# Optimization experiments

Measured on AMD Instinct MI355X. Metric: run time of the kernel, lower is better.

## Reference

```python
import jax, jax.numpy as jnp
import numpy as np

IN_DIM = 512
C_OUT = IN_DIM // 8  # 64
B, H, W = 8, 128, 128


def setup_inputs() -> dict:
    key = jax.random.key(0)
    ks = jax.random.split(key, 6)
    x = jax.random.normal(ks[0], (B, IN_DIM, H, W), dtype=jnp.float32)
    # 1x1 conv weights stored as [out_ch, in_ch] matrices (kernel size 1)
    qkv_w = jax.random.normal(ks[1], (3 * C_OUT, IN_DIM), dtype=jnp.float32) * (1.0 / np.sqrt(IN_DIM))
    qkv_b = jax.random.normal(ks[2], (3 * C_OUT,), dtype=jnp.float32) * 0.01
    out_w = jax.random.normal(ks[3], (IN_DIM, C_OUT), dtype=jnp.float32) * (1.0 / np.sqrt(C_OUT))
    out_b = jax.random.normal(ks[4], (IN_DIM,), dtype=jnp.float32) * 0.01
    # gamma is init to 0 in torch; use a small nonzero value so both paths are exercised
    gamma = jnp.asarray(0.5, dtype=jnp.float32)
    return {"x": x, "qkv_w": qkv_w, "qkv_b": qkv_b, "out_w": out_w, "out_b": out_b, "gamma": gamma}


def reference(x, qkv_w, qkv_b, out_w, out_b, gamma):
    # qkv_conv: 1x1 conv == channel matmul
    qkv = jnp.einsum('bchw,oc->bohw', x, qkv_w) + qkv_b[None, :, None, None]
    q, k, v = jnp.split(qkv, 3, axis=1)  # each [B, C', H, W]

    # Horizontal branch: per column w, channel-channel attention contracting over H
    energy_h = jnp.einsum('bqhw,bkhw->bwqk', q, k)          # [B, W, C', C']
    attn_h = jax.nn.softmax(energy_h, axis=-1)
    out_h = jnp.einsum('bwqk,bkhw->bqhw', attn_h, v)        # [B, C', H, W]

    # Vertical branch: per row h, channel-channel attention contracting over W
    energy_v = jnp.einsum('bqhw,bkhw->bhqk', q, k)          # [B, H, C', C']
    attn_v = jax.nn.softmax(energy_v, axis=-1)
    out_v = jnp.einsum('bhqk,bkhw->bqhw', attn_v, v)        # [B, C', H, W]

    out = gamma * (out_h + out_v)
    out = jnp.einsum('bchw,oc->bohw', out, out_w) + out_b[None, :, None, None]
    return out + x
```

## Files before the change

kernel.cpp:

```cpp
#include <hip/hip_runtime.h>


typedef _Float16 f16;
typedef _Float16 f16x4 __attribute__((ext_vector_type(4)));
typedef _Float16 f16x8 __attribute__((ext_vector_type(8)));
typedef float f32x4 __attribute__((ext_vector_type(4)));

#define MFMA16(a, b, c) __builtin_amdgcn_mfma_f32_16x16x32_f16(a, b, c, 0, 0, 0)

constexpr int CIN = 512;
constexpr int COUT = 64;
constexpr int HW = 128;
constexpr int P = HW * HW;
constexpr int QKV_CH = 192;

__global__ __launch_bounds__(256) void qkv_gemm(
    const float* __restrict__ x, const float* __restrict__ w,
    const float* __restrict__ bias, f16* __restrict__ qkv)
{
  __shared__ __attribute__((aligned(16))) f16 Wl[QKV_CH * 40];
  __shared__ __attribute__((aligned(16))) f16 Xt[128 * 40];
  const int p0 = blockIdx.x * 128;
  const int b = blockIdx.y;
  const float* xb = x + (size_t)b * CIN * P;
  const int t = threadIdx.x;
  const int lane = t & 63, wv = t >> 6;
  const int quad = lane >> 4, l15 = lane & 15;
  const int wm = (wv >> 1) * 32, wn = (wv & 1) * 64;

  f32x4 acc[3][4][2] = {};
  for (int k0 = 0; k0 < CIN; k0 += 32) {
    for (int it = 0; it < 6; ++it) {
      int c = t + it * 256;
      int row = c >> 3, c4 = (c & 7) * 4;
      const float4 v = *(const float4*)(w + (size_t)row * CIN + k0 + c4);
      f16* d = &Wl[row * 40 + c4];
      d[0] = (f16)v.x; d[1] = (f16)v.y; d[2] = (f16)v.z; d[3] = (f16)v.w;
    }
    for (int it = 0; it < 4; ++it) {
      int c = t + it * 256;
      int kr = c >> 5, p4 = (c & 31) * 4;
      const float4 v = *(const float4*)(xb + (size_t)(k0 + kr) * P + p0 + p4);
      float vv[4] = {v.x, v.y, v.z, v.w};
#pragma unroll
      for (int j = 0; j < 4; ++j) {
        int p = p4 + j;
        int kc = kr ^ (((p >> 3) & 3) << 3);
        Xt[p * 40 + kc] = (f16)vv[j];
      }
    }
    __syncthreads();
    f16x8 xf[4];
#pragma unroll
    for (int ps = 0; ps < 4; ++ps) {
      int pr = wn + ps * 16 + l15;
      int kb = (quad * 8) ^ (((pr >> 3) & 3) << 3);
      xf[ps] = *(const f16x8*)&Xt[pr * 40 + kb];
    }
#pragma unroll
    for (int mt = 0; mt < 3; ++mt) {
      f16x8 wf[2];
#pragma unroll
      for (int ms = 0; ms < 2; ++ms)
        wf[ms] = *(const f16x8*)&Wl[(mt * 64 + wm + ms * 16 + l15) * 40 + quad * 8];
#pragma unroll
      for (int ps = 0; ps < 4; ++ps)
#pragma unroll
        for (int ms = 0; ms < 2; ++ms)
          acc[mt][ps][ms] = MFMA16(xf[ps], wf[ms], acc[mt][ps][ms]);
    }
    __syncthreads();
  }
  f16* ob = qkv + (size_t)b * QKV_CH * P;
#pragma unroll
  for (int mt = 0; mt < 3; ++mt) {
#pragma unroll
    for (int ms = 0; ms < 2; ++ms) {
      int m = mt * 64 + wm + ms * 16 + l15;
      float bi = bias[m];
#pragma unroll
      for (int ps = 0; ps < 4; ++ps) {
        int p = p0 + wn + ps * 16 + quad * 4;
        f16x4 tmp;
#pragma unroll
        for (int r = 0; r < 4; ++r) tmp[r] = (f16)(acc[mt][ps][ms][r] + bi);
        *(f16x4*)(ob + (size_t)m * P + p) = tmp;
      }
    }
  }
}

__global__ __launch_bounds__(256) void transpose_hw(
    const f16* __restrict__ in, f16* __restrict__ out)
{
  __shared__ __attribute__((aligned(16))) f16 T[64 * 72];
  const size_t plane = blockIdx.x;
  const int r0 = blockIdx.y * 64, c0 = blockIdx.z * 64;
  const f16* ip = in + plane * P;
  f16* op = out + plane * P;
  const int t = threadIdx.x;
  for (int it = 0; it < 2; ++it) {
    int c = t + it * 256;
    int row = c >> 3, c8 = (c & 7) * 8;
    *(f16x8*)&T[row * 72 + c8] =
        *(const f16x8*)(ip + (size_t)(r0 + row) * HW + c0 + c8);
  }
  __syncthreads();
  for (int it = 0; it < 2; ++it) {
    int c = t + it * 256;
    int wr = c >> 3, h8 = (c & 7) * 8;
    f16 tmp[8];
#pragma unroll
    for (int j = 0; j < 8; ++j) tmp[j] = T[(h8 + j) * 72 + wr];
    *(f16x8*)(op + (size_t)(c0 + wr) * HW + r0 + h8) = *(const f16x8*)tmp;
  }
}

__global__ __launch_bounds__(256, 4) void cc_attn(
    const f16* __restrict__ qkvT, const f16* __restrict__ qkvN,
    f16* __restrict__ outT, f16* __restrict__ outN)
{
  __shared__ __attribute__((aligned(16))) f16 smem[64 * 136 + 128 * 72];
  f16* Kl = smem;
  f16* Vt = smem + 64 * 136;
  f16* Al = smem;
  f16* Ol = smem;
  const int s = blockIdx.x, b = blockIdx.y;
  const f16* src = blockIdx.z ? qkvN : qkvT;
  f16* dst = blockIdx.z ? outN : outT;
  const f16* base = src + (size_t)b * QKV_CH * P + (size_t)s * HW;
  const int t = threadIdx.x;
  const int lane = t & 63, wv = t >> 6;
  const int quad = lane >> 4, l15 = lane & 15;
  const int m0 = wv * 16;

  f16x8 aq[4];
#pragma unroll
  for (int kk = 0; kk < 4; ++kk)
    aq[kk] = *(const f16x8*)(base + (size_t)(m0 + l15) * P + kk * 32 + quad * 8);

  for (int it = 0; it < 4; ++it) {
    int c = t + it * 256;
    int row = c >> 4, c8 = (c & 15) * 8;
    *(f16x8*)&Kl[row * 136 + c8] =
        *(const f16x8*)(base + (size_t)(64 + row) * P + c8);
    f16x8 v = *(const f16x8*)(base + (size_t)(128 + row) * P + c8);
#pragma unroll
    for (int j = 0; j < 8; ++j) {
      int h = c8 + j;
      int kc = row ^ (((h >> 3) & 7) << 3);
      Vt[h * 72 + kc] = v[j];
    }
  }
  __syncthreads();

  f32x4 e[4] = {};
#pragma unroll
  for (int kk = 0; kk < 4; ++kk) {
#pragma unroll
    for (int nt = 0; nt < 4; ++nt) {
      f16x8 bk = *(const f16x8*)&Kl[(nt * 16 + l15) * 136 + kk * 32 + quad * 8];
      e[nt] = MFMA16(aq[kk], bk, e[nt]);
    }
  }
  float pr[4][4];
  float rinv[4];
#pragma unroll
  for (int r = 0; r < 4; ++r) {
    float mx = fmaxf(fmaxf(e[0][r], e[1][r]), fmaxf(e[2][r], e[3][r]));
    for (int off = 1; off < 16; off <<= 1) mx = fmaxf(mx, __shfl_xor(mx, off));
    float sm = 0.f;
#pragma unroll
    for (int nt = 0; nt < 4; ++nt) {
      float pv = __expf(e[nt][r] - mx);
      pr[nt][r] = pv;
      sm += pv;
    }
    for (int off = 1; off < 16; off <<= 1) sm += __shfl_xor(sm, off);
    rinv[r] = 1.0f / sm;
  }
  __syncthreads();

#pragma unroll
  for (int nt = 0; nt < 4; ++nt)
#pragma unroll
    for (int r = 0; r < 4; ++r)
      Al[(m0 + quad * 4 + r) * 72 + nt * 16 + l15] = (f16)(pr[nt][r] * rinv[r]);

  f32x4 o[8] = {};
#pragma unroll
  for (int kk = 0; kk < 2; ++kk) {
    f16x8 ap = *(const f16x8*)&Al[(m0 + l15) * 72 + kk * 32 + quad * 8];
#pragma unroll
    for (int nt = 0; nt < 8; ++nt) {
      int hr = nt * 16 + l15;
      int kb = (kk * 32 + quad * 8) ^ (((hr >> 3) & 7) << 3);
      f16x8 bv = *(const f16x8*)&Vt[hr * 72 + kb];
      o[nt] = MFMA16(ap, bv, o[nt]);
    }
  }
  __syncthreads();

#pragma unroll
  for (int nt = 0; nt < 8; ++nt)
#pragma unroll
    for (int r = 0; r < 4; ++r) {
      int row = m0 + quad * 4 + r;
      int col = nt * 16 + l15;
      Ol[row * 136 + (col ^ ((row & 15) << 3))] = (f16)o[nt][r];
    }
  f16* db = dst + (size_t)b * COUT * P + (size_t)s * HW;
#pragma unroll
  for (int it = 0; it < 4; ++it) {
    int c = lane + it * 64;
    int row = m0 + (c >> 4);
    int c8 = (c & 15) * 8;
    f16x8 vv = *(const f16x8*)&Ol[row * 136 + (c8 ^ ((row & 15) << 3))];
    *(f16x8*)(db + (size_t)row * P + c8) = vv;
  }
}

__global__ __launch_bounds__(256) void out_proj(
    const f16* __restrict__ ah, const f16* __restrict__ av,
    const float* __restrict__ w, const float* __restrict__ bias,
    const float* __restrict__ gamma_p, const float* __restrict__ x,
    float* __restrict__ out)
{
  __shared__ __attribute__((aligned(16))) f16 St[128 * 72];
  const int p0 = blockIdx.x * 128;
  const int b = blockIdx.y;
  const int t = threadIdx.x;
  const int lane = t & 63, wv = t >> 6;
  const int quad = lane >> 4, l15 = lane & 15;
  const int wm = (wv >> 1) * 32, wn = (wv & 1) * 64;

  const size_t abase = (size_t)b * COUT * P + p0;
  for (int it = 0; it < 4; ++it) {
    int c = t + it * 256;
    int k = c >> 4, p8 = (c & 15) * 8;
    f16x8 a = *(const f16x8*)(ah + abase + (size_t)k * P + p8);
    f16x8 vv = *(const f16x8*)(av + abase + (size_t)k * P + p8);
#pragma unroll
    for (int j = 0; j < 8; ++j) {
      int p = p8 + j;
      int kc = k ^ (((p >> 3) & 7) << 3);
      St[p * 72 + kc] = (f16)(a[j] + vv[j]);
    }
  }
  __syncthreads();

  f16x8 sf[2][4];
#pragma unroll
  for (int kk = 0; kk < 2; ++kk)
#pragma unroll
    for (int ps = 0; ps < 4; ++ps) {
      int pr2 = wn + ps * 16 + l15;
      int kb = (kk * 32 + quad * 8) ^ (((pr2 >> 3) & 7) << 3);
      sf[kk][ps] = *(const f16x8*)&St[pr2 * 72 + kb];
    }

  const float g = *gamma_p;
  const float* xb = x + (size_t)b * CIN * P;
  float* ob = out + (size_t)b * CIN * P;

  for (int mt = 0; mt < 8; ++mt) {
    const int m0 = mt * 64;
    f16x8 wf[2][2];
#pragma unroll
    for (int ms = 0; ms < 2; ++ms) {
      const float* wr = w + (size_t)(m0 + wm + ms * 16 + l15) * COUT;
#pragma unroll
      for (int kk = 0; kk < 2; ++kk) {
        const float4 w0 = *(const float4*)(wr + kk * 32 + quad * 8);
        const float4 w1 = *(const float4*)(wr + kk * 32 + quad * 8 + 4);
        f16x8 f;
        f[0] = (f16)w0.x; f[1] = (f16)w0.y; f[2] = (f16)w0.z; f[3] = (f16)w0.w;
        f[4] = (f16)w1.x; f[5] = (f16)w1.y; f[6] = (f16)w1.z; f[7] = (f16)w1.w;
        wf[kk][ms] = f;
      }
    }
    f32x4 acc[4][2] = {};
#pragma unroll
    for (int kk = 0; kk < 2; ++kk)
#pragma unroll
      for (int ps = 0; ps < 4; ++ps)
#pragma unroll
        for (int ms = 0; ms < 2; ++ms)
          acc[ps][ms] = MFMA16(sf[kk][ps], wf[kk][ms], acc[ps][ms]);
#pragma unroll
    for (int ms = 0; ms < 2; ++ms) {
      int m = m0 + wm + ms * 16 + l15;
      float bi = bias[m];
#pragma unroll
      for (int ps = 0; ps < 4; ++ps) {
        int p = p0 + wn + ps * 16 + quad * 4;
        size_t idx = (size_t)m * P + p;
        const float4 xv = *(const float4*)(xb + idx);
        float4 ov;
        ov.x = g * acc[ps][ms][0] + bi + xv.x;
        ov.y = g * acc[ps][ms][1] + bi + xv.y;
        ov.z = g * acc[ps][ms][2] + bi + xv.z;
        ov.w = g * acc[ps][ms][3] + bi + xv.w;
        *(float4*)(ob + idx) = ov;
      }
    }
  }
}

extern "C" void kernel_launch(void* const* d_in, const int* in_sizes, int n_in,
                              void* d_out, int out_size, void* d_ws,
                              size_t ws_size, hipStream_t stream)
{
  (void)in_sizes; (void)n_in; (void)out_size; (void)ws_size;
  const float* x = (const float*)d_in[0];
  const float* qkv_w = (const float*)d_in[1];
  const float* qkv_b = (const float*)d_in[2];
  const float* out_w = (const float*)d_in[3];
  const float* out_b = (const float*)d_in[4];
  const float* gamma = (const float*)d_in[5];
  float* out = (float*)d_out;

  char* ws = (char*)d_ws;
  const size_t QKV_BYTES = (size_t)8 * QKV_CH * P * sizeof(f16);
  const size_t ATT_BYTES = (size_t)8 * COUT * P * sizeof(f16);
  f16* qkv  = (f16*)ws;
  f16* qkvT = (f16*)(ws + QKV_BYTES);
  f16* ahT  = (f16*)(ws + 2 * QKV_BYTES);
  f16* ahN  = (f16*)(ws + 2 * QKV_BYTES + ATT_BYTES);
  f16* avN  = (f16*)(ws + 2 * QKV_BYTES + 2 * ATT_BYTES);

  qkv_gemm<<<dim3(128, 8), 256, 0, stream>>>(x, qkv_w, qkv_b, qkv);
  transpose_hw<<<dim3(8 * QKV_CH, 2, 2), 256, 0, stream>>>(qkv, qkvT);
  cc_attn<<<dim3(128, 8, 2), 256, 0, stream>>>(qkvT, qkv, ahT, avN);
  transpose_hw<<<dim3(8 * COUT, 2, 2), 256, 0, stream>>>(ahT, ahN);
  out_proj<<<dim3(128, 8), 256, 0, stream>>>(ahN, avN, out_w, out_b, gamma,
                                             x, out);
}
```

Baseline: 601.7 us.

## Fuse transposes into QKV GEMM and out-projection, pre-convert weights to fp16

Both standalone transpose kernels are removed. The QKV GEMM now tiles pixels as 8x16 spatial blocks and writes the result in both normal and transposed layouts through a swizzled LDS staging buffer. The out-projection reads the transposed horizontal-branch output directly, also using spatial tiles. Weights are converted to fp16 once in a small prep kernel, and the GEMM register-prefetches the next K slice while computing the current one. This cuts two launches and a full round trip of intermediate tensors through global memory. In exchange it adds strided transposed writes and reads plus extra LDS synchronisation.

```diff
diff --git a/kernel.cpp b/kernel.cpp
--- a/kernel.cpp
+++ b/kernel.cpp
@@ -14,13 +14,33 @@
 constexpr int P = HW * HW;
 constexpr int QKV_CH = 192;
 
+__global__ __launch_bounds__(256) void prep_w(
+    const float* __restrict__ qw, const float* __restrict__ ow,
+    f16* __restrict__ qw16, f16* __restrict__ ow16)
+{
+  int i = blockIdx.x * 256 + threadIdx.x;
+  const float* src;
+  f16* dst;
+  int off;
+  if (i < 24576) { src = qw; dst = qw16; off = i; }
+  else           { src = ow; dst = ow16; off = i - 24576; }
+  const float4 v = *(const float4*)(src + (size_t)off * 4);
+  f16x4 o;
+  o[0] = (f16)v.x; o[1] = (f16)v.y; o[2] = (f16)v.z; o[3] = (f16)v.w;
+  *(f16x4*)(dst + (size_t)off * 4) = o;
+}
+
 __global__ __launch_bounds__(256) void qkv_gemm(
-    const float* __restrict__ x, const float* __restrict__ w,
-    const float* __restrict__ bias, f16* __restrict__ qkv)
-{
-  __shared__ __attribute__((aligned(16))) f16 Wl[QKV_CH * 40];
-  __shared__ __attribute__((aligned(16))) f16 Xt[128 * 40];
-  const int p0 = blockIdx.x * 128;
+    const float* __restrict__ x, const f16* __restrict__ w16,
+    const float* __restrict__ bias, f16* __restrict__ qkv,
+    f16* __restrict__ qkvT)
+{
+  __shared__ __attribute__((aligned(16))) f16 pool[QKV_CH * 40 + 128 * 40];
+  f16* Wl = pool;
+  f16* Xt = pool + QKV_CH * 40;
+  f16* Cl = pool;
+  const int bx = blockIdx.x;
+  const int h0 = (bx >> 3) * 8, w0 = (bx & 7) * 16;
   const int b = blockIdx.y;
   const float* xb = x + (size_t)b * CIN * P;
   const int t = threadIdx.x;
@@ -28,28 +48,46 @@
   const int quad = lane >> 4, l15 = lane & 15;
   const int wm = (wv >> 1) * 32, wn = (wv & 1) * 64;
 
+  f16x8 wvr[3];
+  float4 xvr[4];
+#define LOADW(s)                                                          \
+  _Pragma("unroll") for (int it = 0; it < 3; ++it) {                      \
+    int c = t + it * 256;                                                 \
+    wvr[it] = *(const f16x8*)(w16 + (size_t)(c >> 2) * CIN + (s) * 32 +   \
+                              (c & 3) * 8);                               \
+  }
+#define LOADX(s)                                                          \
+  _Pragma("unroll") for (int it = 0; it < 4; ++it) {                      \
+    int c = t + it * 256;                                                 \
+    int kr = c >> 5, sub = c & 31;                                        \
+    xvr[it] = *(const float4*)(xb + (size_t)((s) * 32 + kr) * P +         \
+                               (h0 + (sub >> 2)) * 128 + w0 + (sub & 3) * 4); \
+  }
+
+  LOADW(0);
+  LOADX(0);
   f32x4 acc[3][4][2] = {};
-  for (int k0 = 0; k0 < CIN; k0 += 32) {
-    for (int it = 0; it < 6; ++it) {
+  for (int s = 0; s < 16; ++s) {
+#pragma unroll
+    for (int it = 0; it < 3; ++it) {
       int c = t + it * 256;
-      int row = c >> 3, c4 = (c & 7) * 4;
-      const float4 v = *(const float4*)(w + (size_t)row * CIN + k0 + c4);
-      f16* d = &Wl[row * 40 + c4];
-      d[0] = (f16)v.x; d[1] = (f16)v.y; d[2] = (f16)v.z; d[3] = (f16)v.w;
-    }
+      *(f16x8*)&Wl[(c >> 2) * 40 + (c & 3) * 8] = wvr[it];
+    }
+#pragma unroll
     for (int it = 0; it < 4; ++it) {
       int c = t + it * 256;
-      int kr = c >> 5, p4 = (c & 31) * 4;
-      const float4 v = *(const float4*)(xb + (size_t)(k0 + kr) * P + p0 + p4);
-      float vv[4] = {v.x, v.y, v.z, v.w};
+      int kr = c >> 5, sub = c & 31;
+      int pb = (sub >> 2) * 16 + (sub & 3) * 4;
+      float vv[4] = {xvr[it].x, xvr[it].y, xvr[it].z, xvr[it].w};
 #pragma unroll
       for (int j = 0; j < 4; ++j) {
-        int p = p4 + j;
+        int p = pb + j;
         int kc = kr ^ (((p >> 3) & 3) << 3);
         Xt[p * 40 + kc] = (f16)vv[j];
       }
     }
     __syncthreads();
+    if (s < 15) { LOADW(s + 1); LOADX(s + 1); }
     f16x8 xf[4];
 #pragma unroll
     for (int ps = 0; ps < 4; ++ps) {
@@ -71,48 +109,53 @@
     }
     __syncthreads();
   }
-  f16* ob = qkv + (size_t)b * QKV_CH * P;
+#undef LOADW
+#undef LOADX
+
+  f16* obN = qkv + (size_t)b * QKV_CH * P;
+  f16* obT = qkvT + (size_t)b * QKV_CH * P;
 #pragma unroll
   for (int mt = 0; mt < 3; ++mt) {
 #pragma unroll
     for (int ms = 0; ms < 2; ++ms) {
-      int m = mt * 64 + wm + ms * 16 + l15;
-      float bi = bias[m];
+      int ml = wm + ms * 16 + l15;
+      float bi = bias[mt * 64 + ml];
 #pragma unroll
       for (int ps = 0; ps < 4; ++ps) {
-        int p = p0 + wn + ps * 16 + quad * 4;
-        f16x4 tmp;
-#pragma unroll
-        for (int r = 0; r < 4; ++r) tmp[r] = (f16)(acc[mt][ps][ms][r] + bi);
-        *(f16x4*)(ob + (size_t)m * P + p) = tmp;
+        int pst = wn + ps * 16 + quad * 4;
+        int col = (((pst >> 3) ^ (ml & 7)) << 3) + (pst & 7);
+        f16x4 tv;
+#pragma unroll
+        for (int r = 0; r < 4; ++r) tv[r] = (f16)(acc[mt][ps][ms][r] + bi);
+        *(f16x4*)&Cl[ml * 136 + col] = tv;
       }
     }
-  }
-}
-
-__global__ __launch_bounds__(256) void transpose_hw(
-    const f16* __restrict__ in, f16* __restrict__ out)
-{
-  __shared__ __attribute__((aligned(16))) f16 T[64 * 72];
-  const size_t plane = blockIdx.x;
-  const int r0 = blockIdx.y * 64, c0 = blockIdx.z * 64;
-  const f16* ip = in + plane * P;
-  f16* op = out + plane * P;
-  const int t = threadIdx.x;
-  for (int it = 0; it < 2; ++it) {
-    int c = t + it * 256;
-    int row = c >> 3, c8 = (c & 7) * 8;
-    *(f16x8*)&T[row * 72 + c8] =
-        *(const f16x8*)(ip + (size_t)(r0 + row) * HW + c0 + c8);
-  }
-  __syncthreads();
-  for (int it = 0; it < 2; ++it) {
-    int c = t + it * 256;
-    int wr = c >> 3, h8 = (c & 7) * 8;
-    f16 tmp[8];
-#pragma unroll
-    for (int j = 0; j < 8; ++j) tmp[j] = T[(h8 + j) * 72 + wr];
-    *(f16x8*)(op + (size_t)(c0 + wr) * HW + r0 + h8) = *(const f16x8*)tmp;
+    __syncthreads();
+#pragma unroll
+    for (int it = 0; it < 4; ++it) {
+      int c = t + it * 256;
+      int ml = c >> 4, sub = c & 15;
+      int hh = sub >> 1, w8 = (sub & 1) * 8;
+      int pst = hh * 16 + w8;
+      int col = (((pst >> 3) ^ (ml & 7)) << 3);
+      f16x8 rd = *(const f16x8*)&Cl[ml * 136 + col];
+      *(f16x8*)(obN + (size_t)(mt * 64 + ml) * P + (h0 + hh) * 128 + w0 + w8) = rd;
+    }
+#pragma unroll
+    for (int it = 0; it < 4; ++it) {
+      int c = t + it * 256;
+      int ml = c >> 4, ww = c & 15;
+      f16 tmp[8];
+#pragma unroll
+      for (int hh = 0; hh < 8; ++hh) {
+        int p = hh * 16 + ww;
+        int col = (((p >> 3) ^ (ml & 7)) << 3) + (p & 7);
+        tmp[hh] = Cl[ml * 136 + col];
+      }
+      *(f16x8*)(obT + (size_t)(mt * 64 + ml) * P + (size_t)(w0 + ww) * 128 + h0) =
+          *(const f16x8*)tmp;
+    }
+    __syncthreads();
   }
 }
 
@@ -221,30 +264,42 @@
 }
 
 __global__ __launch_bounds__(256) void out_proj(
-    const f16* __restrict__ ah, const f16* __restrict__ av,
-    const float* __restrict__ w, const float* __restrict__ bias,
+    const f16* __restrict__ ahT, const f16* __restrict__ av,
+    const f16* __restrict__ w16, const float* __restrict__ bias,
     const float* __restrict__ gamma_p, const float* __restrict__ x,
     float* __restrict__ out)
 {
   __shared__ __attribute__((aligned(16))) f16 St[128 * 72];
-  const int p0 = blockIdx.x * 128;
+  const int bx = blockIdx.x;
+  const int h0 = (bx >> 3) * 8, w0 = (bx & 7) * 16;
   const int b = blockIdx.y;
   const int t = threadIdx.x;
   const int lane = t & 63, wv = t >> 6;
   const int quad = lane >> 4, l15 = lane & 15;
   const int wm = (wv >> 1) * 32, wn = (wv & 1) * 64;
 
-  const size_t abase = (size_t)b * COUT * P + p0;
+  const size_t abase = (size_t)b * COUT * P;
   for (int it = 0; it < 4; ++it) {
     int c = t + it * 256;
-    int k = c >> 4, p8 = (c & 15) * 8;
-    f16x8 a = *(const f16x8*)(ah + abase + (size_t)k * P + p8);
-    f16x8 vv = *(const f16x8*)(av + abase + (size_t)k * P + p8);
+    int k = c >> 4, sub = c & 15;
+    int hh = sub >> 1, w8 = (sub & 1) * 8;
+    f16x8 vv = *(const f16x8*)(av + abase + (size_t)k * P + (h0 + hh) * 128 + w0 + w8);
 #pragma unroll
     for (int j = 0; j < 8; ++j) {
-      int p = p8 + j;
-      int kc = k ^ (((p >> 3) & 7) << 3);
-      St[p * 72 + kc] = (f16)(a[j] + vv[j]);
+      int p = hh * 16 + w8 + j;
+      St[p * 72 + (k ^ (((p >> 3) & 7) << 3))] = vv[j];
+    }
+  }
+  __syncthreads();
+  for (int it = 0; it < 4; ++it) {
+    int c = t + it * 256;
+    int k = c >> 4, ww = c & 15;
+    f16x8 vv = *(const f16x8*)(ahT + abase + (size_t)k * P + (size_t)(w0 + ww) * 128 + h0);
+#pragma unroll
+    for (int j = 0; j < 8; ++j) {
+      int p = j * 16 + ww;
+      int idx = p * 72 + (k ^ (((p >> 3) & 7) << 3));
+      St[idx] = St[idx] + vv[j];
     }
   }
   __syncthreads();
@@ -268,16 +323,10 @@
     f16x8 wf[2][2];
 #pragma unroll
     for (int ms = 0; ms < 2; ++ms) {
-      const float* wr = w + (size_t)(m0 + wm + ms * 16 + l15) * COUT;
-#pragma unroll
-      for (int kk = 0; kk < 2; ++kk) {
-        const float4 w0 = *(const float4*)(wr + kk * 32 + quad * 8);
-        const float4 w1 = *(const float4*)(wr + kk * 32 + quad * 8 + 4);
-        f16x8 f;
-        f[0] = (f16)w0.x; f[1] = (f16)w0.y; f[2] = (f16)w0.z; f[3] = (f16)w0.w;
-        f[4] = (f16)w1.x; f[5] = (f16)w1.y; f[6] = (f16)w1.z; f[7] = (f16)w1.w;
-        wf[kk][ms] = f;
-      }
+      const f16* wr = w16 + (size_t)(m0 + wm + ms * 16 + l15) * COUT;
+#pragma unroll
+      for (int kk = 0; kk < 2; ++kk)
+        wf[kk][ms] = *(const f16x8*)(wr + kk * 32 + quad * 8);
     }
     f32x4 acc[4][2] = {};
 #pragma unroll
@@ -293,8 +342,9 @@
       float bi = bias[m];
 #pragma unroll
       for (int ps = 0; ps < 4; ++ps) {
-        int p = p0 + wn + ps * 16 + quad * 4;
-        size_t idx = (size_t)m * P + p;
+        int pst = wn + ps * 16 + quad * 4;
+        int hh = pst >> 4, ww = pst & 15;
+        size_t idx = (size_t)m * P + (h0 + hh) * 128 + w0 + ww;
         const float4 xv = *(const float4*)(xb + idx);
         float4 ov;
         ov.x = g * acc[ps][ms][0] + bi + xv.x;
@@ -326,13 +376,13 @@
   f16* qkv  = (f16*)ws;
   f16* qkvT = (f16*)(ws + QKV_BYTES);
   f16* ahT  = (f16*)(ws + 2 * QKV_BYTES);
-  f16* ahN  = (f16*)(ws + 2 * QKV_BYTES + ATT_BYTES);
-  f16* avN  = (f16*)(ws + 2 * QKV_BYTES + 2 * ATT_BYTES);
-
-  qkv_gemm<<<dim3(128, 8), 256, 0, stream>>>(x, qkv_w, qkv_b, qkv);
-  transpose_hw<<<dim3(8 * QKV_CH, 2, 2), 256, 0, stream>>>(qkv, qkvT);
+  f16* avN  = (f16*)(ws + 2 * QKV_BYTES + ATT_BYTES);
+  f16* wq16 = (f16*)(ws + 2 * QKV_BYTES + 2 * ATT_BYTES);
+  f16* wo16 = wq16 + (size_t)QKV_CH * CIN;
+
+  prep_w<<<dim3(128), 256, 0, stream>>>(qkv_w, out_w, wq16, wo16);
+  qkv_gemm<<<dim3(128, 8), 256, 0, stream>>>(x, wq16, qkv_b, qkv, qkvT);
   cc_attn<<<dim3(128, 8, 2), 256, 0, stream>>>(qkvT, qkv, ahT, avN);
-  transpose_hw<<<dim3(8 * COUT, 2, 2), 256, 0, stream>>>(ahT, ahN);
-  out_proj<<<dim3(128, 8), 256, 0, stream>>>(ahN, avN, out_w, out_b, gamma,
+  out_proj<<<dim3(128, 8), 256, 0, stream>>>(ahT, avN, wo16, out_b, gamma,
                                              x, out);
 }
```

Measured after the change: 656.9 us. 1.09x slower.

## Pre-convert weights to fp16, prefetch qkv_gemm tiles, shrink out_proj tiles

Applied to the files above, without the earlier changes.

Adds a small kernel that converts both weight matrices to fp16 once per call, so the GEMMs load half-width weights and skip per-tile conversion. qkv_gemm now register-prefetches the next K-slice of weights and x while MFMAs run on the current slice (software pipelining). out_proj is retiled to 64 pixels per block with each wave owning 16 output rows, doubling the grid and setting launch bounds for more occupancy. The cost is an extra kernel launch, some extra workspace, and higher register pressure in qkv_gemm.

```diff
diff --git a/kernel.cpp b/kernel.cpp
--- a/kernel.cpp
+++ b/kernel.cpp
@@ -14,8 +14,24 @@
 constexpr int P = HW * HW;
 constexpr int QKV_CH = 192;
 
+__global__ __launch_bounds__(256) void prep_w(
+    const float* __restrict__ qw, const float* __restrict__ ow,
+    f16* __restrict__ qw16, f16* __restrict__ ow16)
+{
+  int i = blockIdx.x * 256 + threadIdx.x;
+  const float* src;
+  f16* dst;
+  int off;
+  if (i < 24576) { src = qw; dst = qw16; off = i; }
+  else           { src = ow; dst = ow16; off = i - 24576; }
+  const float4 v = *(const float4*)(src + (size_t)off * 4);
+  f16x4 o;
+  o[0] = (f16)v.x; o[1] = (f16)v.y; o[2] = (f16)v.z; o[3] = (f16)v.w;
+  *(f16x4*)(dst + (size_t)off * 4) = o;
+}
+
 __global__ __launch_bounds__(256) void qkv_gemm(
-    const float* __restrict__ x, const float* __restrict__ w,
+    const float* __restrict__ x, const f16* __restrict__ w16,
     const float* __restrict__ bias, f16* __restrict__ qkv)
 {
   __shared__ __attribute__((aligned(16))) f16 Wl[QKV_CH * 40];
@@ -28,20 +44,35 @@
   const int quad = lane >> 4, l15 = lane & 15;
   const int wm = (wv >> 1) * 32, wn = (wv & 1) * 64;
 
+  f16x8 wvr[3];
+  float4 xvr[4];
+#define LOADW(s)                                                          \
+  _Pragma("unroll") for (int it = 0; it < 3; ++it) {                      \
+    int c = t + it * 256;                                                 \
+    wvr[it] = *(const f16x8*)(w16 + (size_t)(c >> 2) * CIN + (s) * 32 +   \
+                              (c & 3) * 8);                               \
+  }
+#define LOADX(s)                                                          \
+  _Pragma("unroll") for (int it = 0; it < 4; ++it) {                      \
+    int c = t + it * 256;                                                 \
+    xvr[it] = *(const float4*)(xb + (size_t)((s) * 32 + (c >> 5)) * P +   \
+                               p0 + (c & 31) * 4);                        \
+  }
+
+  LOADW(0);
+  LOADX(0);
   f32x4 acc[3][4][2] = {};
-  for (int k0 = 0; k0 < CIN; k0 += 32) {
-    for (int it = 0; it < 6; ++it) {
+  for (int s = 0; s < 16; ++s) {
+#pragma unroll
+    for (int it = 0; it < 3; ++it) {
       int c = t + it * 256;
-      int row = c >> 3, c4 = (c & 7) * 4;
-      const float4 v = *(const float4*)(w + (size_t)row * CIN + k0 + c4);
-      f16* d = &Wl[row * 40 + c4];
-      d[0] = (f16)v.x; d[1] = (f16)v.y; d[2] = (f16)v.z; d[3] = (f16)v.w;
-    }
+      *(f16x8*)&Wl[(c >> 2) * 40 + (c & 3) * 8] = wvr[it];
+    }
+#pragma unroll
     for (int it = 0; it < 4; ++it) {
       int c = t + it * 256;
       int kr = c >> 5, p4 = (c & 31) * 4;
-      const float4 v = *(const float4*)(xb + (size_t)(k0 + kr) * P + p0 + p4);
-      float vv[4] = {v.x, v.y, v.z, v.w};
+      float vv[4] = {xvr[it].x, xvr[it].y, xvr[it].z, xvr[it].w};
 #pragma unroll
       for (int j = 0; j < 4; ++j) {
         int p = p4 + j;
@@ -50,6 +81,7 @@
       }
     }
     __syncthreads();
+    if (s < 15) { LOADW(s + 1); LOADX(s + 1); }
     f16x8 xf[4];
 #pragma unroll
     for (int ps = 0; ps < 4; ++ps) {
@@ -71,6 +103,9 @@
     }
     __syncthreads();
   }
+#undef LOADW
+#undef LOADX
+
   f16* ob = qkv + (size_t)b * QKV_CH * P;
 #pragma unroll
   for (int mt = 0; mt < 3; ++mt) {
@@ -220,31 +255,29 @@
   }
 }
 
-__global__ __launch_bounds__(256) void out_proj(
+__global__ __launch_bounds__(256, 5) void out_proj(
     const f16* __restrict__ ah, const f16* __restrict__ av,
-    const float* __restrict__ w, const float* __restrict__ bias,
+    const f16* __restrict__ w16, const float* __restrict__ bias,
     const float* __restrict__ gamma_p, const float* __restrict__ x,
     float* __restrict__ out)
 {
-  __shared__ __attribute__((aligned(16))) f16 St[128 * 72];
-  const int p0 = blockIdx.x * 128;
+  __shared__ __attribute__((aligned(16))) f16 St[64 * 72];
+  const int p0 = blockIdx.x * 64;
   const int b = blockIdx.y;
   const int t = threadIdx.x;
   const int lane = t & 63, wv = t >> 6;
   const int quad = lane >> 4, l15 = lane & 15;
-  const int wm = (wv >> 1) * 32, wn = (wv & 1) * 64;
 
   const size_t abase = (size_t)b * COUT * P + p0;
-  for (int it = 0; it < 4; ++it) {
+  for (int it = 0; it < 2; ++it) {
     int c = t + it * 256;
-    int k = c >> 4, p8 = (c & 15) * 8;
+    int k = c >> 3, p8 = (c & 7) * 8;
     f16x8 a = *(const f16x8*)(ah + abase + (size_t)k * P + p8);
     f16x8 vv = *(const f16x8*)(av + abase + (size_t)k * P + p8);
 #pragma unroll
     for (int j = 0; j < 8; ++j) {
       int p = p8 + j;
-      int kc = k ^ (((p >> 3) & 7) << 3);
-      St[p * 72 + kc] = (f16)(a[j] + vv[j]);
+      St[p * 72 + (k ^ (((p >> 3) & 7) << 3))] = (f16)(a[j] + vv[j]);
     }
   }
   __syncthreads();
@@ -254,7 +287,7 @@
   for (int kk = 0; kk < 2; ++kk)
 #pragma unroll
     for (int ps = 0; ps < 4; ++ps) {
-      int pr2 = wn + ps * 16 + l15;
+      int pr2 = ps * 16 + l15;
       int kb = (kk * 32 + quad * 8) ^ (((pr2 >> 3) & 7) << 3);
       sf[kk][ps] = *(const f16x8*)&St[pr2 * 72 + kb];
     }
@@ -264,45 +297,29 @@
   float* ob = out + (size_t)b * CIN * P;
 
   for (int mt = 0; mt < 8; ++mt) {
-    const int m0 = mt * 64;
-    f16x8 wf[2][2];
-#pragma unroll
-    for (int ms = 0; ms < 2; ++ms) {
-      const float* wr = w + (size_t)(m0 + wm + ms * 16 + l15) * COUT;
-#pragma unroll
-      for (int kk = 0; kk < 2; ++kk) {
-        const float4 w0 = *(const float4*)(wr + kk * 32 + quad * 8);
-        const float4 w1 = *(const float4*)(wr + kk * 32 + quad * 8 + 4);
-        f16x8 f;
-        f[0] = (f16)w0.x; f[1] = (f16)w0.y; f[2] = (f16)w0.z; f[3] = (f16)w0.w;
-        f[4] = (f16)w1.x; f[5] = (f16)w1.y; f[6] = (f16)w1.z; f[7] = (f16)w1.w;
-        wf[kk][ms] = f;
-      }
-    }
-    f32x4 acc[4][2] = {};
+    const int m = mt * 64 + wv * 16 + l15;
+    f16x8 wf[2];
 #pragma unroll
     for (int kk = 0; kk < 2; ++kk)
+      wf[kk] = *(const f16x8*)(w16 + (size_t)m * COUT + kk * 32 + quad * 8);
+    f32x4 acc[4] = {};
+#pragma unroll
+    for (int kk = 0; kk < 2; ++kk)
 #pragma unroll
       for (int ps = 0; ps < 4; ++ps)
-#pragma unroll
-        for (int ms = 0; ms < 2; ++ms)
-          acc[ps][ms] = MFMA16(sf[kk][ps], wf[kk][ms], acc[ps][ms]);
-#pragma unroll
-    for (int ms = 0; ms < 2; ++ms) {
-      int m = m0 + wm + ms * 16 + l15;
-      float bi = bias[m];
-#pragma unroll
-      for (int ps = 0; ps < 4; ++ps) {
-        int p = p0 + wn + ps * 16 + quad * 4;
-        size_t idx = (size_t)m * P + p;
-        const float4 xv = *(const float4*)(xb + idx);
-        float4 ov;
-        ov.x = g * acc[ps][ms][0] + bi + xv.x;
-        ov.y = g * acc[ps][ms][1] + bi + xv.y;
-        ov.z = g * acc[ps][ms][2] + bi + xv.z;
-        ov.w = g * acc[ps][ms][3] + bi + xv.w;
-        *(float4*)(ob + idx) = ov;
-      }
+        acc[ps] = MFMA16(sf[kk][ps], wf[kk], acc[ps]);
+    float bi = bias[m];
+#pragma unroll
+    for (int ps = 0; ps < 4; ++ps) {
+      int p = p0 + ps * 16 + quad * 4;
+      size_t idx = (size_t)m * P + p;
+      const float4 xv = *(const float4*)(xb + idx);
+      float4 ov;
+      ov.x = g * acc[ps][0] + bi + xv.x;
+      ov.y = g * acc[ps][1] + bi + xv.y;
+      ov.z = g * acc[ps][2] + bi + xv.z;
+      ov.w = g * acc[ps][3] + bi + xv.w;
+      *(float4*)(ob + idx) = ov;
     }
   }
 }
@@ -328,11 +345,14 @@
   f16* ahT  = (f16*)(ws + 2 * QKV_BYTES);
   f16* ahN  = (f16*)(ws + 2 * QKV_BYTES + ATT_BYTES);
   f16* avN  = (f16*)(ws + 2 * QKV_BYTES + 2 * ATT_BYTES);
-
-  qkv_gemm<<<dim3(128, 8), 256, 0, stream>>>(x, qkv_w, qkv_b, qkv);
+  f16* wq16 = (f16*)(ws + 2 * QKV_BYTES + 3 * ATT_BYTES);
+  f16* wo16 = wq16 + (size_t)QKV_CH * CIN;
+
+  prep_w<<<dim3(128), 256, 0, stream>>>(qkv_w, out_w, wq16, wo16);
+  qkv_gemm<<<dim3(128, 8), 256, 0, stream>>>(x, wq16, qkv_b, qkv);
   transpose_hw<<<dim3(8 * QKV_CH, 2, 2), 256, 0, stream>>>(qkv, qkvT);
   cc_attn<<<dim3(128, 8, 2), 256, 0, stream>>>(qkvT, qkv, ahT, avN);
   transpose_hw<<<dim3(8 * COUT, 2, 2), 256, 0, stream>>>(ahT, ahN);
-  out_proj<<<dim3(128, 8), 256, 0, stream>>>(ahN, avN, out_w, out_b, gamma,
+  out_proj<<<dim3(256, 8), 256, 0, stream>>>(ahN, avN, wo16, out_b, gamma,
                                              x, out);
 }
```

Result: no change. 600.8 us (-0.1%).
